# Kernel tuning notes

Hardware: AMD Instinct MI355X
Metric: run time of the kernel (lower is better)

## Reference

```python
import jax, jax.numpy as jnp
import numpy as np

B = 32          # batch size
N = 32          # image dim -> P = N*N points per sample
P = N * N
F = 64          # point feature dim (= MLP output)
K = 32          # max_neighbors
R = 0.1         # ball-query radius
EPS = 1e-5      # batchnorm eps


def setup_inputs() -> dict:
    key = jax.random.key(0)
    ks = jax.random.split(key, 4)
    NP = B * P
    x = jax.random.normal(ks[0], (NP, F), jnp.float32)
    pos = jax.random.uniform(ks[1], (NP, 2), jnp.float32)
    # module requires exactly N*N points per sample, sorted by batch
    batch = jnp.repeat(jnp.arange(B, dtype=jnp.int32), P)
    # MLP([66,128,64]) params: Linear->BN->ReLU->Linear
    W1 = jax.random.normal(ks[2], (F + 2, 128), jnp.float32) * (1.0 / np.sqrt(F + 2))
    b1 = jnp.zeros((128,), jnp.float32)
    gamma1 = jnp.ones((128,), jnp.float32)
    beta1 = jnp.zeros((128,), jnp.float32)
    W2 = jax.random.normal(ks[3], (128, F), jnp.float32) * (1.0 / np.sqrt(128))
    b2 = jnp.zeros((F,), jnp.float32)
    return {"x": x, "pos": pos, "batch": batch, "W1": W1, "b1": b1,
            "gamma1": gamma1, "beta1": beta1, "W2": W2, "b2": b2}


def reference(x, pos, batch, W1, b1, gamma1, beta1, W2, b2):
    NP = x.shape[0]
    posb = pos.reshape(B, P, 2)
    # pixel (target) index of every query point: batch*N*N + row*N + col
    rows = jnp.clip((pos[:, 1] * N).astype(jnp.int32), 0, N - 1)
    cols = jnp.clip((pos[:, 0] * N).astype(jnp.int32), 0, N - 1)
    pix = batch.astype(jnp.int32) * (N * N) + rows * N + cols          # [NP]
    # radius ball query within each batch sample (deterministic: nearest-K within R)
    d2 = jnp.sum((posb[:, :, None, :] - posb[:, None, :, :]) ** 2, -1)  # [B,P,P]
    d2 = jnp.where(d2 <= R * R, d2, jnp.inf)
    negd, nbr = jax.lax.top_k(-d2, K)                                   # [B,P,K]
    valid = jnp.isfinite(negd)
    src = (jnp.arange(B, dtype=jnp.int32)[:, None, None] * P + nbr).reshape(-1)  # [B*P*K]
    dst = jnp.broadcast_to(pix.reshape(B, P)[:, :, None], (B, P, K)).reshape(-1)
    mask = valid.reshape(-1) & (src != dst)          # remove_self_loops
    # PointNetConv message: concat(x_j, pos_j - pos_i); pos_i indexed by mapped target
    relpos = pos[src] - pos[dst]
    msg_nb = jnp.concatenate([x[src], relpos], -1)                    # [B*P*K, F+2]
    # add_self_loops: edge (i, i) for every node -> relpos = 0
    msg_self = jnp.concatenate([x, jnp.zeros_like(pos)], -1)          # [NP, F+2]
    msg = jnp.concatenate([msg_nb, msg_self], 0)
    m = jnp.concatenate([mask, jnp.ones((NP,), bool)], 0)
    tgt = jnp.concatenate([dst, jnp.arange(NP, dtype=jnp.int32)], 0)
    # MLP: Linear -> BatchNorm(training stats over valid messages) -> ReLU -> Linear
    z = msg @ W1 + b1
    mf = m.astype(z.dtype)[:, None]
    cnt = jnp.sum(mf)
    mean = jnp.sum(z * mf, 0, keepdims=True) / cnt
    var = jnp.sum(((z - mean) ** 2) * mf, 0, keepdims=True) / cnt
    h = jax.nn.relu((z - mean) / jnp.sqrt(var + EPS) * gamma1 + beta1)
    o = h @ W2 + b2                                                    # [M, F]
    # scatter-max aggregation into B*N*N pixel nodes (self loops make all nonempty)
    o = jnp.where(m[:, None], o, -jnp.inf)
    pixel_features = jax.ops.segment_max(o, tgt, num_segments=NP)
    images = pixel_features.reshape(B, N, N, F).transpose(0, 3, 1, 2)
    return images
```

## Files before the change

### kernel.cpp

```cpp
#include <hip/hip_runtime.h>
#include <hip/hip_bf16.h>
#include <math.h>


#define NPTS   32768
#define KNB    32
#define BN_EPS 1e-5f

#define WS_NBRS     0u
#define WS_NBRCNT   4194304u
#define WS_DEG      4325376u
#define WS_STX      4456448u
#define WS_STY      4587520u
#define WS_DEFREP   4718592u
#define WS_SCSH     4719616u
#define WS_W2B      4720640u
#define WS_PART     4737024u
#define WS_Y        5265408u
#define WS_SCRATCH  5265408u
#define WS_BQPART   13654016u
#define WS_WB       13654016u
#define WS_QCNT     22042624u
#define WS_QSTART   22173696u
#define WS_QLIST    22304768u
#define WS_ISLOT    22435840u
#define WS_SELF     22566912u
#define WS_SHP      30955520u

typedef __attribute__((ext_vector_type(8))) short short8;
typedef __attribute__((ext_vector_type(4))) float floatx4;

__device__ __forceinline__ unsigned short f2bf(float f) {
    unsigned int u = __float_as_uint(f);
    unsigned int r = u + 0x7fffu + ((u >> 16) & 1u);
    return (unsigned short)(r >> 16);
}
__device__ __forceinline__ float bf_lo(unsigned int w) { return __uint_as_float(w << 16); }
__device__ __forceinline__ float bf_hi(unsigned int w) { return __uint_as_float(w & 0xffff0000u); }
__device__ __forceinline__ unsigned int pack_bf2(float lo, float hi) {
    __hip_bfloat162 hh = __float22bfloat162_rn(make_float2(lo, hi));
    return *reinterpret_cast<unsigned int*>(&hh);
}

__launch_bounds__(256)
__global__ void k_prep(const float* __restrict__ W2, unsigned short* __restrict__ w2b,
                       float* __restrict__ defrep, const float* __restrict__ pos,
                       int* __restrict__ qcnt, int* __restrict__ qstart,
                       int* __restrict__ qlist, int* __restrict__ islot) {
    int tid = threadIdx.x;
    int gt = blockIdx.x * 256 + tid;
    if (gt < 256) defrep[gt] = 0.0f;
    {
        int j  = gt & 7;
        int L  = (gt >> 3) & 63;
        int ks = (gt >> 9) & 3;
        int t4 = gt >> 11;
        int k = ks * 32 + (L >> 4) * 8 + j;
        int n = t4 * 16 + (L & 15);
        w2b[gt] = f2bf(W2[k * 64 + n]);
    }
    __shared__ int cntS[1024], preS[1024], offS[1024], pixOf[1024];
    __shared__ int wtot[4];
    int s = blockIdx.x;
    int base = s << 10;
    for (int i = tid; i < 1024; i += 256) cntS[i] = 0;
    __syncthreads();
    for (int ql = tid; ql < 1024; ql += 256) {
        float2 p = *(const float2*)&pos[2 * (base + ql)];
        int row = min(max((int)(p.y * 32.0f), 0), 31);
        int col = min(max((int)(p.x * 32.0f), 0), 31);
        int pixl = row * 32 + col;
        pixOf[ql] = pixl;
        atomicAdd(&cntS[pixl], 1);
    }
    __syncthreads();
    int a0 = cntS[4 * tid], a1 = cntS[4 * tid + 1], a2 = cntS[4 * tid + 2], a3 = cntS[4 * tid + 3];
    int tsum = a0 + a1 + a2 + a3;
    int lane = tid & 63, wv = tid >> 6;
    int v = tsum;
    for (int o = 1; o < 64; o <<= 1) { int u = __shfl_up(v, o); if (lane >= o) v += u; }
    if (lane == 63) wtot[wv] = v;
    __syncthreads();
    int wbase = 0;
    for (int w = 0; w < wv; ++w) wbase += wtot[w];
    int excl = wbase + v - tsum;
    preS[4 * tid] = excl;
    preS[4 * tid + 1] = excl + a0;
    preS[4 * tid + 2] = excl + a0 + a1;
    preS[4 * tid + 3] = excl + a0 + a1 + a2;
    __syncthreads();
    for (int i = tid; i < 1024; i += 256) offS[i] = preS[i];
    __syncthreads();
    for (int ql = tid; ql < 1024; ql += 256) {
        int p = pixOf[ql];
        int slot = atomicAdd(&offS[p], 1);
        qlist[base + slot] = base + ql;
        islot[base + ql] = base + slot;
    }
    for (int i = tid; i < 1024; i += 256) {
        qcnt[base + i] = cntS[i];
        qstart[base + i] = base + preS[i];
    }
}

__launch_bounds__(256)
__global__ void k_ballquery(const float* __restrict__ pos,
                            int* __restrict__ nbrs, int* __restrict__ nbr_cnt,
                            float* __restrict__ bqpart, float* __restrict__ defrep) {
    __shared__ float2 poss[1024];
    __shared__ float accd[1024], accx[1024], accy[1024];
    __shared__ unsigned long long cand[4][256];
    __shared__ int cnt[4], ocnt[4];
    int tid = threadIdx.x, wave = tid >> 6, lane = tid & 63;
    int s = blockIdx.x >> 4;
    int chunk = blockIdx.x & 15;
    int base = s << 10;
    for (int i = tid; i < 1024; i += 256) poss[i] = *(const float2*)&pos[2 * (base + i)];
    for (int i = tid; i < 1024; i += 256) { accd[i] = 0.0f; accx[i] = 0.0f; accy[i] = 0.0f; }
    __syncthreads();
    float2 pr[16];
#pragma unroll
    for (int k = 0; k < 16; ++k) pr[k] = poss[k * 64 + lane];

    float aD = 0, aE = 0, aF = 0;
    for (int qi = 0; qi < 16; ++qi) {
        int ql = chunk * 64 + wave * 16 + qi;
        int q = base + ql;
        float2 qp = poss[ql];
        int row = min(max((int)(qp.y * 32.0f), 0), 31);
        int col = min(max((int)(qp.x * 32.0f), 0), 31);
        int pixl = row * 32 + col;
        float2 tp = poss[pixl];
        if (lane == 0) { cnt[wave] = 0; ocnt[wave] = 0; }
        __builtin_amdgcn_wave_barrier();
#pragma unroll
        for (int k = 0; k < 16; ++k) {
            float dx = pr[k].x - qp.x, dy = pr[k].y - qp.y;
            float d2 = __fadd_rn(__fmul_rn(dx, dx), __fmul_rn(dy, dy));
            if (d2 <= 0.01f) {
                int sl = atomicAdd(&cnt[wave], 1);
                if (sl < 256)
                    cand[wave][sl] = ((unsigned long long)__float_as_uint(d2) << 32)
                                     | (unsigned int)(k * 64 + lane);
            }
        }
        __builtin_amdgcn_wave_barrier();
        int c = min(cnt[wave], 256);
        for (int i = lane; i < c; i += 64) {
            unsigned long long key = cand[wave][i];
            int rank = 0;
            for (int t = 0; t < c; ++t) rank += (cand[wave][t] < key) ? 1 : 0;
            int j = (int)(key & 0xffffffffu);
            if (rank < KNB && j != pixl) {
                int sl = atomicAdd(&ocnt[wave], 1);
                nbrs[q * KNB + sl] = base + j;
                float rx = poss[j].x - tp.x, ry = poss[j].y - tp.y;
                aD += rx * rx; aE += rx * ry; aF += ry * ry;
                atomicAdd(&accd[j], 1.0f);
                atomicAdd(&accx[j], tp.x);
                atomicAdd(&accy[j], tp.y);
            }
        }
        __builtin_amdgcn_wave_barrier();
        if (lane == 0) nbr_cnt[q] = ocnt[wave];
    }
#pragma unroll
    for (int o = 1; o < 64; o <<= 1) {
        aD += __shfl_xor(aD, o); aE += __shfl_xor(aE, o); aF += __shfl_xor(aF, o);
    }
    __syncthreads();
    float* pb = &bqpart[blockIdx.x * 3072];
    for (int i = tid; i < 1024; i += 256) {
        pb[i] = accd[i]; pb[1024 + i] = accx[i]; pb[2048 + i] = accy[i];
    }
    if (tid == 0) {
        int r = (blockIdx.x & 63) * 4;
        atomicAdd(&defrep[r + 0], aD);
        atomicAdd(&defrep[r + 1], aE);
        atomicAdd(&defrep[r + 2], aF);
    }
}

__global__ void k_nodeagg(const float* __restrict__ bqpart, float* __restrict__ deg,
                          float* __restrict__ stx, float* __restrict__ sty) {
    int t = blockIdx.x * 256 + threadIdx.x;
    int s = t >> 10, off = t & 1023;
    const float* pb = &bqpart[(s * 16) * 3072];
    float d = 0, xx = 0, yy = 0;
    for (int j = 0; j < 16; ++j) {
        d  += pb[j * 3072 + off];
        xx += pb[j * 3072 + 1024 + off];
        yy += pb[j * 3072 + 2048 + off];
    }
    deg[t] = d; stx[t] = xx; sty[t] = yy;
}

__launch_bounds__(256)
__global__ void k_y(const float* __restrict__ x, const float* __restrict__ W1,
                    const float* __restrict__ b1, const float* __restrict__ pos,
                    const float* __restrict__ deg, const float* __restrict__ stxA,
                    const float* __restrict__ styA,
                    unsigned int* __restrict__ yb, float* __restrict__ partials) {
    __shared__ float w1s[64 * 128];
    __shared__ float stage[4][512];
    __shared__ float lsum[515];
    int tid = threadIdx.x;
    for (int i = tid; i < 64 * 128; i += 256) w1s[i] = W1[i];
    for (int i = tid; i < 515; i += 256) lsum[i] = 0.0f;
    __syncthreads();
    int wave = tid >> 6, lane = tid & 63;
    int f0 = 2 * lane, f1 = 2 * lane + 1;
    float b10 = b1[f0], b11 = b1[f1];
    float* st = &stage[wave][0];
    float P0 = 0, Q0 = 0, R0 = 0, S0 = 0, P1 = 0, Q1 = 0, R1 = 0, S1 = 0;
    float sB = 0, sC = 0, sDeg = 0;

    for (int it = 0; it < 4; ++it) {
        int nbase = ((blockIdx.x * 4 + wave) * 4 + it) * 8;
        __builtin_amdgcn_wave_barrier();
#pragma unroll
        for (int mm = 0; mm < 8; ++mm)
            st[mm * 64 + lane] = x[(nbase + mm) * 64 + lane];
        __builtin_amdgcn_wave_barrier();
        float z0[8], z1[8];
#pragma unroll
        for (int mm = 0; mm < 8; ++mm) { z0[mm] = b10; z1[mm] = b11; }
        for (int k4 = 0; k4 < 16; ++k4) {
            float2 wv0 = *(const float2*)&w1s[(k4 * 4 + 0) * 128 + f0];
            float2 wv1 = *(const float2*)&w1s[(k4 * 4 + 1) * 128 + f0];
            float2 wv2 = *(const float2*)&w1s[(k4 * 4 + 2) * 128 + f0];
            float2 wv3 = *(const float2*)&w1s[(k4 * 4 + 3) * 128 + f0];
#pragma unroll
            for (int mm = 0; mm < 8; ++mm) {
                float4 mk = *(const float4*)&st[mm * 64 + k4 * 4];
                z0[mm] += mk.x * wv0.x + mk.y * wv1.x + mk.z * wv2.x + mk.w * wv3.x;
                z1[mm] += mk.x * wv0.y + mk.y * wv1.y + mk.z * wv2.y + mk.w * wv3.y;
            }
        }
#pragma unroll
        for (int mm = 0; mm < 8; ++mm) {
            int n = nbase + mm;
            float dg = deg[n];
            float wgt = 1.0f + dg;
            float Bn = dg * pos[2 * n]     - stxA[n];
            float Cn = dg * pos[2 * n + 1] - styA[n];
            float a = z0[mm], bq = z1[mm];
            P0 += wgt * a;  Q0 += wgt * a * a;  R0 += a * Bn;  S0 += a * Cn;
            P1 += wgt * bq; Q1 += wgt * bq * bq; R1 += bq * Bn; S1 += bq * Cn;
            sB += Bn; sC += Cn; sDeg += dg;
            yb[n * 64 + lane] = pack_bf2(a, bq);
        }
    }
    atomicAdd(&lsum[f0], P0);        atomicAdd(&lsum[f1], P1);
    atomicAdd(&lsum[128 + f0], Q0);  atomicAdd(&lsum[128 + f1], Q1);
    atomicAdd(&lsum[256 + f0], R0);  atomicAdd(&lsum[256 + f1], R1);
    atomicAdd(&lsum[384 + f0], S0);  atomicAdd(&lsum[384 + f1], S1);
    if (lane == 0) {
        atomicAdd(&lsum[512], sB);
        atomicAdd(&lsum[513], sC);
        atomicAdd(&lsum[514], sDeg);
    }
    __syncthreads();
    for (int i = tid; i < 515; i += 256) partials[blockIdx.x * 516 + i] = lsum[i];
}

__global__ void k_finalize(const float* __restrict__ gamma, const float* __restrict__ beta,
                           const float* __restrict__ W1, const float* __restrict__ partials,
                           const float* __restrict__ defrep, float* __restrict__ scsh) {
    __shared__ float red[515];
    __shared__ float sDEF[3];
    int tid = threadIdx.x;
    for (int i = tid; i < 515; i += 256) {
        float s = 0;
        for (int b = 0; b < 256; ++b) s += partials[b * 516 + i];
        red[i] = s;
    }
    if (tid < 3) {
        float s = 0;
        for (int r = 0; r < 64; ++r) s += defrep[r * 4 + tid];
        sDEF[tid] = s;
    }
    __syncthreads();
    if (tid < 128) {
        int f = tid;
        float P = red[f], Q = red[128 + f], R = red[256 + f], S = red[384 + f];
        float SB = red[512], SC = red[513], SDeg = red[514];
        float u = W1[8192 + f], v = W1[8320 + f];
        float cntv = 32768.0f + SDeg;
        float mean = (P + u * SB + v * SC) / cntv;
        float E2 = (Q + 2.0f * u * R + 2.0f * v * S
                    + u * u * sDEF[0] + 2.0f * u * v * sDEF[1] + v * v * sDEF[2]) / cntv;
        float var = E2 - mean * mean;
        float sc = gamma[f] / sqrtf(var + BN_EPS);
        scsh[f] = sc;
        scsh[128 + f] = beta[f] - mean * sc;
    }
}

__launch_bounds__(256)
__global__ void k_self(const unsigned int* __restrict__ yb, const float* __restrict__ pos,
                       const float* __restrict__ W1, const float* __restrict__ scsh,
                       const unsigned short* __restrict__ w2b, const float* __restrict__ b2,
                       unsigned int* __restrict__ wbuf, unsigned int* __restrict__ shpbuf,
                       float* __restrict__ selfbuf, float* __restrict__ out) {
    __shared__ unsigned short hbuf[4][16 * 136];
    int tid = threadIdx.x, wave = tid >> 6, lane = tid & 63;
    unsigned short* hb = hbuf[wave];
    short8 bfrag[4][4];
#pragma unroll
    for (int t = 0; t < 4; ++t)
#pragma unroll
        for (int ks = 0; ks < 4; ++ks)
            bfrag[t][ks] = *(const short8*)&w2b[((t * 4 + ks) * 64 + lane) * 8];
    int f0 = 2 * lane;
    float sc0 = scsh[f0],     sh0 = scsh[128 + f0];
    float sc1 = scsh[f0 + 1], sh1 = scsh[129 + f0];
    float u0 = W1[8192 + f0], v0 = W1[8320 + f0];
    float u1 = W1[8193 + f0], v1 = W1[8321 + f0];
    float b2v0 = b2[(lane & 15)],      b2v1 = b2[16 + (lane & 15)];
    float b2v2 = b2[32 + (lane & 15)], b2v3 = b2[48 + (lane & 15)];

    int nbase = (blockIdx.x * 4 + wave) * 16;
#pragma unroll
    for (int c = 0; c < 2; ++c) {
        unsigned int yw[8];
#pragma unroll
        for (int j = 0; j < 8; ++j)
            yw[j] = yb[(nbase + c * 8 + j) * 64 + lane];
#pragma unroll
        for (int j = 0; j < 8; ++j) {
            int e = c * 8 + j;
            int nn = nbase + e;
            float y0 = bf_lo(yw[j]), y1 = bf_hi(yw[j]);
            float h0 = fmaxf(y0 * sc0 + sh0, 0.0f);
            float h1 = fmaxf(y1 * sc1 + sh1, 0.0f);
            *(unsigned int*)&hb[e * 136 + f0] = pack_bf2(h0, h1);
            float px = pos[2 * nn], py = pos[2 * nn + 1];
            float ts0 = (px * u0 + py * v0) * sc0;
            float ts1 = (px * u1 + py * v1) * sc1;
            wbuf[nn * 64 + lane]   = pack_bf2(y0 * sc0 + ts0, y1 * sc1 + ts1);
            shpbuf[nn * 64 + lane] = pack_bf2(sh0 - ts0, sh1 - ts1);
        }
    }
    __builtin_amdgcn_wave_barrier();
    floatx4 acc0 = {0,0,0,0}, acc1 = {0,0,0,0}, acc2 = {0,0,0,0}, acc3 = {0,0,0,0};
#pragma unroll
    for (int ks = 0; ks < 4; ++ks) {
        short8 a = *(const short8*)&hb[(lane & 15) * 136 + ks * 32 + (lane >> 4) * 8];
        acc0 = __builtin_amdgcn_mfma_f32_16x16x32_bf16(a, bfrag[0][ks], acc0, 0, 0, 0);
        acc1 = __builtin_amdgcn_mfma_f32_16x16x32_bf16(a, bfrag[1][ks], acc1, 0, 0, 0);
        acc2 = __builtin_amdgcn_mfma_f32_16x16x32_bf16(a, bfrag[2][ks], acc2, 0, 0, 0);
        acc3 = __builtin_amdgcn_mfma_f32_16x16x32_bf16(a, bfrag[3][ks], acc3, 0, 0, 0);
    }
    int nrow = nbase + (lane >> 4) * 4;
#pragma unroll
    for (int r = 0; r < 4; ++r) {
        int n = nrow + r;
        int obase = (n >> 10) * 65536 + (n & 1023);
        float o0 = acc0[r] + b2v0, o1 = acc1[r] + b2v1;
        float o2 = acc2[r] + b2v2, o3 = acc3[r] + b2v3;
        out[obase + ((lane & 15)) * 1024]      = o0;
        out[obase + (16 + (lane & 15)) * 1024] = o1;
        out[obase + (32 + (lane & 15)) * 1024] = o2;
        out[obase + (48 + (lane & 15)) * 1024] = o3;
        selfbuf[n * 64 + (lane & 15)]      = o0;
        selfbuf[n * 64 + 16 + (lane & 15)] = o1;
        selfbuf[n * 64 + 32 + (lane & 15)] = o2;
        selfbuf[n * 64 + 48 + (lane & 15)] = o3;
    }
}

__launch_bounds__(256)
__global__ void k_out(const unsigned int* __restrict__ wbuf,
                      const unsigned int* __restrict__ shpbuf,
                      const float* __restrict__ pos,
                      const unsigned short* __restrict__ w2b, const float* __restrict__ b2,
                      const int* __restrict__ nbrs, const int* __restrict__ nbr_cnt,
                      const int* __restrict__ islot, float* __restrict__ scratch) {
    int tid = threadIdx.x, wave = tid >> 6, lane = tid & 63;
    short8 bfrag[4][4];
#pragma unroll
    for (int t = 0; t < 4; ++t)
#pragma unroll
        for (int ks = 0; ks < 4; ++ks)
            bfrag[t][ks] = *(const short8*)&w2b[((t * 4 + ks) * 64 + lane) * 8];
    float b2l = b2[lane];
    int em = lane & 15;
    int koff = (lane >> 4) * 4;
    int wid = blockIdx.x * 4 + wave;

    for (int qi = 0; qi < 2; ++qi) {
        int q = wid * 2 + qi;
        int m = nbr_cnt[q];
        int b = q >> 10;
        float qx = pos[2 * q], qy = pos[2 * q + 1];
        int row = min(max((int)(qy * 32.0f), 0), 31);
        int col = min(max((int)(qx * 32.0f), 0), 31);
        int pixq = (b << 10) + row * 32 + col;
        uint4 sv0 = *(const uint4*)&shpbuf[pixq * 64 + 0 * 16 + koff];
        uint4 sv1 = *(const uint4*)&shpbuf[pixq * 64 + 1 * 16 + koff];
        uint4 sv2 = *(const uint4*)&shpbuf[pixq * 64 + 2 * 16 + koff];
        uint4 sv3 = *(const uint4*)&shpbuf[pixq * 64 + 3 * 16 + koff];
        int nv = (lane < m) ? nbrs[q * KNB + lane] : 0;
        float om0[4], om1[4], om2[4], om3[4];
#pragma unroll
        for (int r = 0; r < 4; ++r) { om0[r] = -INFINITY; om1[r] = -INFINITY; om2[r] = -INFINITY; om3[r] = -INFINITY; }

        for (int mt = 0; mt * 16 < m; ++mt) {
            int src = __shfl(nv, mt * 16 + em);
            const unsigned int* wp = &wbuf[src * 64 + koff];
            floatx4 a0 = {0,0,0,0}, a1 = {0,0,0,0}, a2 = {0,0,0,0}, a3 = {0,0,0,0};
#pragma unroll
            for (int ks = 0; ks < 4; ++ks) {
                uint4 wv = *(const uint4*)&wp[ks * 16];
                uint4 sv = (ks == 0) ? sv0 : (ks == 1) ? sv1 : (ks == 2) ? sv2 : sv3;
                union { unsigned int u[4]; short8 s8; } af;
#pragma unroll
                for (int qd = 0; qd < 4; ++qd) {
                    unsigned int wd = (qd == 0) ? wv.x : (qd == 1) ? wv.y : (qd == 2) ? wv.z : wv.w;
                    unsigned int sd = (qd == 0) ? sv.x : (qd == 1) ? sv.y : (qd == 2) ? sv.z : sv.w;
                    float lo = fmaxf(bf_lo(wd) + bf_lo(sd), 0.0f);
                    float hi = fmaxf(bf_hi(wd) + bf_hi(sd), 0.0f);
                    af.u[qd] = pack_bf2(lo, hi);
                }
                a0 = __builtin_amdgcn_mfma_f32_16x16x32_bf16(af.s8, bfrag[0][ks], a0, 0, 0, 0);
                a1 = __builtin_amdgcn_mfma_f32_16x16x32_bf16(af.s8, bfrag[1][ks], a1, 0, 0, 0);
                a2 = __builtin_amdgcn_mfma_f32_16x16x32_bf16(af.s8, bfrag[2][ks], a2, 0, 0, 0);
                a3 = __builtin_amdgcn_mfma_f32_16x16x32_bf16(af.s8, bfrag[3][ks], a3, 0, 0, 0);
            }
            int rowb = (lane >> 4) * 4;
#pragma unroll
            for (int r = 0; r < 4; ++r) {
                int e = mt * 16 + rowb + r;
                if (e < m) {
                    om0[r] = fmaxf(om0[r], a0[r]);
                    om1[r] = fmaxf(om1[r], a1[r]);
                    om2[r] = fmaxf(om2[r], a2[r]);
                    om3[r] = fmaxf(om3[r], a3[r]);
                }
            }
        }
        float w0 = fmaxf(fmaxf(om0[0], om0[1]), fmaxf(om0[2], om0[3]));
        float w1 = fmaxf(fmaxf(om1[0], om1[1]), fmaxf(om1[2], om1[3]));
        float w2 = fmaxf(fmaxf(om2[0], om2[1]), fmaxf(om2[2], om2[3]));
        float w3 = fmaxf(fmaxf(om3[0], om3[1]), fmaxf(om3[2], om3[3]));
        w0 = fmaxf(w0, __shfl_xor(w0, 16)); w0 = fmaxf(w0, __shfl_xor(w0, 32));
        w1 = fmaxf(w1, __shfl_xor(w1, 16)); w1 = fmaxf(w1, __shfl_xor(w1, 32));
        w2 = fmaxf(w2, __shfl_xor(w2, 16)); w2 = fmaxf(w2, __shfl_xor(w2, 32));
        w3 = fmaxf(w3, __shfl_xor(w3, 16)); w3 = fmaxf(w3, __shfl_xor(w3, 32));
        int g4 = lane >> 4;
        float vf = (g4 == 0) ? w0 : (g4 == 1) ? w1 : (g4 == 2) ? w2 : w3;
        vf += b2l;
        scratch[islot[q] * 64 + lane] = vf;
    }
}

__launch_bounds__(256)
__global__ void k_gather(const float* __restrict__ scratch, const float* __restrict__ selfbuf,
                         const int* __restrict__ qcnt, const int* __restrict__ qstart,
                         float* __restrict__ out) {
    int tid = threadIdx.x, wave = tid >> 6, lane = tid & 63;
    int n = blockIdx.x * 4 + wave;
    int c = qcnt[n];
    if (c == 0) return;
    int qs = qstart[n];
    float v = selfbuf[n * 64 + lane];
    for (int i = 0; i < c; ++i)
        v = fmaxf(v, scratch[(qs + i) * 64 + lane]);
    out[(n >> 10) * 65536 + lane * 1024 + (n & 1023)] = v;
}

extern "C" void kernel_launch(void* const* d_in, const int* in_sizes, int n_in,
                              void* d_out, int out_size, void* d_ws, size_t ws_size,
                              hipStream_t stream) {
    const float* x     = (const float*)d_in[0];
    const float* pos   = (const float*)d_in[1];
    const float* W1    = (const float*)d_in[3];
    const float* b1    = (const float*)d_in[4];
    const float* gamma = (const float*)d_in[5];
    const float* beta  = (const float*)d_in[6];
    const float* W2    = (const float*)d_in[7];
    const float* b2    = (const float*)d_in[8];
    float* out = (float*)d_out;
    char* ws = (char*)d_ws;
    int*   nbrs     = (int*)(ws + WS_NBRS);
    int*   nbr_cnt  = (int*)(ws + WS_NBRCNT);
    float* deg      = (float*)(ws + WS_DEG);
    float* stx      = (float*)(ws + WS_STX);
    float* sty      = (float*)(ws + WS_STY);
    float* defrep   = (float*)(ws + WS_DEFREP);
    float* scsh     = (float*)(ws + WS_SCSH);
    unsigned short* w2b = (unsigned short*)(ws + WS_W2B);
    float* partials = (float*)(ws + WS_PART);
    unsigned int* yb = (unsigned int*)(ws + WS_Y);
    float* scratch  = (float*)(ws + WS_SCRATCH);
    float* bqpart   = (float*)(ws + WS_BQPART);
    unsigned int* wbuf = (unsigned int*)(ws + WS_WB);
    int* qcnt   = (int*)(ws + WS_QCNT);
    int* qstart = (int*)(ws + WS_QSTART);
    int* qlist  = (int*)(ws + WS_QLIST);
    int* islot  = (int*)(ws + WS_ISLOT);
    float* selfbuf = (float*)(ws + WS_SELF);
    unsigned int* shpbuf = (unsigned int*)(ws + WS_SHP);

    k_prep<<<32, 256, 0, stream>>>(W2, w2b, defrep, pos, qcnt, qstart, qlist, islot);
    k_ballquery<<<512, 256, 0, stream>>>(pos, nbrs, nbr_cnt, bqpart, defrep);
    k_nodeagg<<<128, 256, 0, stream>>>(bqpart, deg, stx, sty);
    k_y<<<256, 256, 0, stream>>>(x, W1, b1, pos, deg, stx, sty, yb, partials);
    k_finalize<<<1, 256, 0, stream>>>(gamma, beta, W1, partials, defrep, scsh);
    k_self<<<NPTS / 64, 256, 0, stream>>>(yb, pos, W1, scsh, w2b, b2, wbuf, shpbuf, selfbuf, out);
    k_out<<<NPTS / 8, 256, 0, stream>>>(wbuf, shpbuf, pos, w2b, b2,
                                        nbrs, nbr_cnt, islot, scratch);
    k_gather<<<NPTS / 4, 256, 0, stream>>>(scratch, selfbuf, qcnt, qstart, out);
}
```

Baseline: 276.3 us.

## Use ballot-based compaction in ball query, skip ranking when few candidates, double grid

Replaces LDS atomic slot allocation for candidates and selected neighbours with wave ballot plus popcount prefix compaction. When a query has no more than K candidates, the O(c^2) rank computation is skipped. The ball-query grid doubles to 1024 blocks of 8 queries per wave, which spreads the work more widely but doubles the per-block partial buffers. That buffer is moved to a larger workspace region, and k_nodeagg now reduces 32 partials per sample instead of 16.

Result: faster. 249.4 us (-9.7%).

```diff
diff --git a/kernel.cpp b/kernel.cpp
--- a/kernel.cpp
+++ b/kernel.cpp
@@ -18,7 +18,6 @@
 #define WS_PART     4737024u
 #define WS_Y        5265408u
 #define WS_SCRATCH  5265408u
-#define WS_BQPART   13654016u
 #define WS_WB       13654016u
 #define WS_QCNT     22042624u
 #define WS_QSTART   22173696u
@@ -26,6 +25,7 @@
 #define WS_ISLOT    22435840u
 #define WS_SELF     22566912u
 #define WS_SHP      30955520u
+#define WS_BQPART   22566912u
 
 typedef __attribute__((ext_vector_type(8))) short short8;
 typedef __attribute__((ext_vector_type(4))) float floatx4;
@@ -110,10 +110,9 @@
     __shared__ float2 poss[1024];
     __shared__ float accd[1024], accx[1024], accy[1024];
     __shared__ unsigned long long cand[4][256];
-    __shared__ int cnt[4], ocnt[4];
     int tid = threadIdx.x, wave = tid >> 6, lane = tid & 63;
-    int s = blockIdx.x >> 4;
-    int chunk = blockIdx.x & 15;
+    int s = blockIdx.x >> 5;
+    int chunk = blockIdx.x & 31;
     int base = s << 10;
     for (int i = tid; i < 1024; i += 256) poss[i] = *(const float2*)&pos[2 * (base + i)];
     for (int i = tid; i < 1024; i += 256) { accd[i] = 0.0f; accx[i] = 0.0f; accy[i] = 0.0f; }
@@ -121,48 +120,64 @@
     float2 pr[16];
 #pragma unroll
     for (int k = 0; k < 16; ++k) pr[k] = poss[k * 64 + lane];
+    unsigned long long lb = (1ull << lane) - 1ull;
 
     float aD = 0, aE = 0, aF = 0;
-    for (int qi = 0; qi < 16; ++qi) {
-        int ql = chunk * 64 + wave * 16 + qi;
+    for (int qi = 0; qi < 8; ++qi) {
+        int ql = chunk * 32 + wave * 8 + qi;
         int q = base + ql;
         float2 qp = poss[ql];
         int row = min(max((int)(qp.y * 32.0f), 0), 31);
         int col = min(max((int)(qp.x * 32.0f), 0), 31);
         int pixl = row * 32 + col;
         float2 tp = poss[pixl];
-        if (lane == 0) { cnt[wave] = 0; ocnt[wave] = 0; }
+        int cnt = 0;
         __builtin_amdgcn_wave_barrier();
 #pragma unroll
         for (int k = 0; k < 16; ++k) {
             float dx = pr[k].x - qp.x, dy = pr[k].y - qp.y;
             float d2 = __fadd_rn(__fmul_rn(dx, dx), __fmul_rn(dy, dy));
-            if (d2 <= 0.01f) {
-                int sl = atomicAdd(&cnt[wave], 1);
-                if (sl < 256)
-                    cand[wave][sl] = ((unsigned long long)__float_as_uint(d2) << 32)
-                                     | (unsigned int)(k * 64 + lane);
+            bool pred = (d2 <= 0.01f);
+            unsigned long long mask = __ballot(pred);
+            if (pred) {
+                int slot = cnt + (int)__popcll(mask & lb);
+                if (slot < 256)
+                    cand[wave][slot] = ((unsigned long long)__float_as_uint(d2) << 32)
+                                       | (unsigned int)(k * 64 + lane);
             }
+            cnt += (int)__popcll(mask);
         }
+        cnt = min(cnt, 256);
         __builtin_amdgcn_wave_barrier();
-        int c = min(cnt[wave], 256);
-        for (int i = lane; i < c; i += 64) {
-            unsigned long long key = cand[wave][i];
-            int rank = 0;
-            for (int t = 0; t < c; ++t) rank += (cand[wave][t] < key) ? 1 : 0;
-            int j = (int)(key & 0xffffffffu);
-            if (rank < KNB && j != pixl) {
-                int sl = atomicAdd(&ocnt[wave], 1);
-                nbrs[q * KNB + sl] = base + j;
+        int osel = 0;
+        for (int cb = 0; cb < cnt; cb += 64) {
+            int i = cb + lane;
+            bool sel = false;
+            int j = 0;
+            if (i < cnt) {
+                unsigned long long key = cand[wave][i];
+                j = (int)(key & 0xffffffffu);
+                if (cnt <= KNB) {
+                    sel = (j != pixl);
+                } else {
+                    int rank = 0;
+                    for (int t = 0; t < cnt; ++t) rank += (cand[wave][t] < key) ? 1 : 0;
+                    sel = (rank < KNB) && (j != pixl);
+                }
+            }
+            unsigned long long mask = __ballot(sel);
+            if (sel) {
+                int slot = osel + (int)__popcll(mask & lb);
+                nbrs[q * KNB + slot] = base + j;
                 float rx = poss[j].x - tp.x, ry = poss[j].y - tp.y;
                 aD += rx * rx; aE += rx * ry; aF += ry * ry;
                 atomicAdd(&accd[j], 1.0f);
                 atomicAdd(&accx[j], tp.x);
                 atomicAdd(&accy[j], tp.y);
             }
+            osel += (int)__popcll(mask);
         }
-        __builtin_amdgcn_wave_barrier();
-        if (lane == 0) nbr_cnt[q] = ocnt[wave];
+        if (lane == 0) nbr_cnt[q] = osel;
     }
 #pragma unroll
     for (int o = 1; o < 64; o <<= 1) {
@@ -185,9 +200,9 @@
                           float* __restrict__ stx, float* __restrict__ sty) {
     int t = blockIdx.x * 256 + threadIdx.x;
     int s = t >> 10, off = t & 1023;
-    const float* pb = &bqpart[(s * 16) * 3072];
+    const float* pb = &bqpart[(s * 32) * 3072];
     float d = 0, xx = 0, yy = 0;
-    for (int j = 0; j < 16; ++j) {
+    for (int j = 0; j < 32; ++j) {
         d  += pb[j * 3072 + off];
         xx += pb[j * 3072 + 1024 + off];
         yy += pb[j * 3072 + 2048 + off];
@@ -494,7 +509,6 @@
     float* partials = (float*)(ws + WS_PART);
     unsigned int* yb = (unsigned int*)(ws + WS_Y);
     float* scratch  = (float*)(ws + WS_SCRATCH);
-    float* bqpart   = (float*)(ws + WS_BQPART);
     unsigned int* wbuf = (unsigned int*)(ws + WS_WB);
     int* qcnt   = (int*)(ws + WS_QCNT);
     int* qstart = (int*)(ws + WS_QSTART);
@@ -502,9 +516,10 @@
     int* islot  = (int*)(ws + WS_ISLOT);
     float* selfbuf = (float*)(ws + WS_SELF);
     unsigned int* shpbuf = (unsigned int*)(ws + WS_SHP);
+    float* bqpart   = (float*)(ws + WS_BQPART);
 
     k_prep<<<32, 256, 0, stream>>>(W2, w2b, defrep, pos, qcnt, qstart, qlist, islot);
-    k_ballquery<<<512, 256, 0, stream>>>(pos, nbrs, nbr_cnt, bqpart, defrep);
+    k_ballquery<<<1024, 256, 0, stream>>>(pos, nbrs, nbr_cnt, bqpart, defrep);
     k_nodeagg<<<128, 256, 0, stream>>>(bqpart, deg, stx, sty);
     k_y<<<256, 256, 0, stream>>>(x, W1, b1, pos, deg, stx, sty, yb, partials);
     k_finalize<<<1, 256, 0, stream>>>(gamma, beta, W1, partials, defrep, scsh);
```
